# Performance work log

Hardware: AMD Instinct MI355X
Metric: run time of the kernel (lower is better)

The kernel has to match this reference:

```python
import jax, jax.numpy as jnp
import numpy as np

B, N, X, H = 128, 1023, 256, 256  # N = 2**(D+1)-1 perfect binary trees, root at 0


def _lin_init(key, out_d, in_d, scale=None):
    if scale is None:
        scale = 1.0 / np.sqrt(in_d)
    kw, kb = jax.random.split(key)
    W = jax.random.uniform(kw, (out_d, in_d), jnp.float32, -scale, scale)
    b = jax.random.uniform(kb, (out_d,), jnp.float32, -scale, scale)
    return W, b


def setup_inputs() -> dict:
    key = jax.random.key(0)
    ks = jax.random.split(key, 16)
    embed = jax.random.normal(ks[0], (B, N, X), jnp.float32)
    Wf, bf = _lin_init(ks[1], H, X + H)
    Wi, bi = _lin_init(ks[2], H, X + H)
    Wu, bu = _lin_init(ks[3], H, X + H)
    Wo, bo = _lin_init(ks[4], H, X + H)
    # extra nn.Parameter biases, initialized to zeros as in the module
    b_f = jnp.zeros((H,), jnp.float32)
    b_i = jnp.zeros((H,), jnp.float32)
    b_u = jnp.zeros((H,), jnp.float32)
    b_o = jnp.zeros((H,), jnp.float32)
    W1, bl1 = _lin_init(ks[5], H, H)
    W2, bl2 = _lin_init(ks[6], H, H)
    W3, bl3 = _lin_init(ks[7], H, H)
    W4, bl4 = _lin_init(ks[8], H, H)
    return {"embed": embed, "Wf": Wf, "bf": bf, "b_f": b_f, "Wi": Wi, "bi": bi,
            "b_i": b_i, "Wu": Wu, "bu": bu, "b_u": b_u, "Wo": Wo, "bo": bo,
            "b_o": b_o, "W1": W1, "bl1": bl1, "W2": W2, "bl2": bl2,
            "W3": W3, "bl3": bl3, "W4": W4, "bl4": bl4}


def _tree_lstm(embed, Wf, bf, b_f, Wi, bi, b_i, Wu, bu, b_u, Wo, bo, b_o):
    Bn, Nn, Xn = embed.shape
    Hn = Wf.shape[0]
    D = int(np.log2(Nn + 1)) - 1  # leaf level index
    h = jnp.zeros((Bn, Nn, Hn), embed.dtype)
    c = jnp.zeros((Bn, Nn, Hn), embed.dtype)
    # initial (leaf) level: no children -> h_sum = 0, c_tilde = 0 (apply_node_func on init state)
    i_g = jax.nn.sigmoid(bi + b_i)
    u_g = jnp.tanh(bu + b_u)
    c_leaf = i_g * u_g
    h_leaf = jax.nn.sigmoid(bo + b_o) * jnp.tanh(c_leaf)
    ls, lc = 2 ** D - 1, 2 ** D
    h = h.at[:, ls:ls + lc].set(jnp.broadcast_to(h_leaf, (Bn, lc, Hn)))
    c = c.at[:, ls:ls + lc].set(jnp.broadcast_to(c_leaf, (Bn, lc, Hn)))
    # level-by-level leaf->root; children of node n are 2n+1, 2n+2 (contiguous per level)
    for l in range(D - 1, -1, -1):
        s, cnt = 2 ** l - 1, 2 ** l
        cs, ccnt = 2 ** (l + 1) - 1, 2 ** (l + 1)
        ch_h = h[:, cs:cs + ccnt]        # [B, 2*cnt, H]
        ch_c = c[:, cs:cs + ccnt]
        ch_e = embed[:, cs:cs + ccnt]
        # message: cat([h, embed]); reduce: sum over the 2 children
        msg = jnp.concatenate([ch_h, ch_e], axis=-1).reshape(Bn, cnt, 2, Hn + Xn)
        h_sum = msg.sum(axis=2)                                   # [B, cnt, H+X]
        c_sum = ch_c.reshape(Bn, cnt, 2, Hn).sum(axis=2)          # [B, cnt, H]
        f = jax.nn.sigmoid(h_sum @ Wf.T + bf + b_f)
        c_tilde = f * c_sum  # f broadcast over children: f*(c1+c2) == sum_k f*c_k
        i_gate = jax.nn.sigmoid(h_sum @ Wi.T + bi + b_i)
        u = jnp.tanh(h_sum @ Wu.T + bu + b_u)
        c_new = i_gate * u + c_tilde
        o = jax.nn.sigmoid(h_sum @ Wo.T + bo + b_o)
        h_new = o * jnp.tanh(c_new)
        h = h.at[:, s:s + cnt].set(h_new)
        c = c.at[:, s:s + cnt].set(c_new)
    return h[:, 0]  # root hidden state, [B, H]


def reference(embed, Wf, bf, b_f, Wi, bi, b_i, Wu, bu, b_u, Wo, bo, b_o,
              W1, bl1, W2, bl2, W3, bl3, W4, bl4):
    hr = _tree_lstm(embed, Wf, bf, b_f, Wi, bi, b_i, Wu, bu, b_u, Wo, bo, b_o)
    # dropout is identity in eval mode
    y = jnp.tanh(hr @ W1.T + bl1)
    y2 = jax.nn.relu(hr @ W2.T + bl2) @ W3.T + bl3
    return jax.nn.relu((y + y2) @ W4.T + bl4)
```

## Files before the change

kernel.cpp:

```cpp
#include <hip/hip_runtime.h>

#define HD 256
#define KD 512

typedef _Float16 half8 __attribute__((ext_vector_type(8)));
typedef _Float16 half2v __attribute__((ext_vector_type(2)));
typedef _Float16 half4v __attribute__((ext_vector_type(4)));
typedef float floatx4 __attribute__((ext_vector_type(4)));
typedef float floatx2 __attribute__((ext_vector_type(2)));

__device__ __forceinline__ float sigmf_(float x) { return 1.f / (1.f + __expf(-x)); }
__device__ __forceinline__ float tanhf_(float x) {
  x = fminf(fmaxf(x, -15.f), 15.f);
  float e = __expf(2.f * x);
  return (e - 1.f) / (e + 1.f);
}

__global__ void prep_kernel(const float* __restrict__ bf_, const float* __restrict__ b_f,
                            const float* __restrict__ bi_, const float* __restrict__ b_i,
                            const float* __restrict__ bu_, const float* __restrict__ b_u,
                            const float* __restrict__ bo_, const float* __restrict__ b_o,
                            const float* __restrict__ Wf, const float* __restrict__ Wi,
                            const float* __restrict__ Wu, const float* __restrict__ Wo,
                            float* __restrict__ bsum, float* __restrict__ bias2,
                            float* __restrict__ cleaf2)
{
  __shared__ float hl2[HD];
  __shared__ float part[64][4];
  const int t = threadIdx.x;
  float sf = bf_[t] + b_f[t];
  float si = bi_[t] + b_i[t];
  float su = bu_[t] + b_u[t];
  float so = bo_[t] + b_o[t];
  float ig = 1.f / (1.f + expf(-si));
  float uu = tanhf(su);
  float cl = ig * uu;
  float hl = (1.f / (1.f + expf(-so))) * tanhf(cl);
  hl2[t] = 2.f * hl;
  if (blockIdx.x == 0) {
    bsum[t] = sf; bsum[HD + t] = si; bsum[2 * HD + t] = su; bsum[3 * HD + t] = so;
    cleaf2[t] = cl + cl;
  }
  __syncthreads();
  const int g = blockIdx.x >> 2, q = blockIdx.x & 3;
  const int nl = t >> 2, kq = t & 3;
  const float* Wg = (g == 0) ? Wf : (g == 1) ? Wi : (g == 2) ? Wu : Wo;
  const float* w = Wg + (long)(q * 64 + nl) * KD + kq * 64;
  float s = 0.f;
  for (int k = 0; k < 64; k += 4) {
    floatx4 wv = *(const floatx4*)(w + k);
    floatx4 hv = *(const floatx4*)(&hl2[kq * 64 + k]);
    s += wv[0] * hv[0] + wv[1] * hv[1] + wv[2] * hv[2] + wv[3] * hv[3];
  }
  part[nl][kq] = s;
  __syncthreads();
  if (kq == 0) {
    const int n = q * 64 + nl;
    float tot = part[nl][0] + part[nl][1] + part[nl][2] + part[nl][3];
    float bg = (g == 0) ? (bf_[n] + b_f[n]) : (g == 1) ? (bi_[n] + b_i[n])
             : (g == 2) ? (bu_[n] + b_u[n]) : (bo_[n] + b_o[n]);
    bias2[g * HD + n] = bg + tot;
  }
}

__global__ void wcvt_kernel(const float* __restrict__ Wf, const float* __restrict__ Wi,
                            const float* __restrict__ Wu, const float* __restrict__ Wo,
                            _Float16* __restrict__ Wh)
{
  int idx = (blockIdx.x * 256 + threadIdx.x) * 4;
  int g = idx >> 17;
  int rem = idx & ((1 << 17) - 1);
  const float* src = (g == 0) ? Wf : (g == 1) ? Wi : (g == 2) ? Wu : Wo;
  floatx4 v = *(const floatx4*)(src + rem);
  half4v o;
  o[0] = (_Float16)v[0]; o[1] = (_Float16)v[1]; o[2] = (_Float16)v[2]; o[3] = (_Float16)v[3];
  *(half4v*)(Wh + idx) = o;
}

__global__ void esum_kernel(const float* __restrict__ embed, _Float16* __restrict__ esum)
{
  const int task = blockIdx.x * 256 + threadIdx.x;
  if (task >= 511 * 32) return;
  const int b = blockIdx.y;
  const int p = task >> 5, g8 = task & 31;
  const float* e0 = embed + ((long)b * 1023 + 2 * p + 1) * 256 + g8 * 8;
  const float* e1 = e0 + 256;
  floatx4 x0 = *(const floatx4*)(e0);
  floatx4 x1 = *(const floatx4*)(e0 + 4);
  floatx4 y0 = *(const floatx4*)(e1);
  floatx4 y1 = *(const floatx4*)(e1 + 4);
  half8 s;
#pragma unroll
  for (int e = 0; e < 4; ++e) { s[e] = (_Float16)(x0[e] + y0[e]); s[4 + e] = (_Float16)(x1[e] + y1[e]); }
  *(half8*)(esum + ((long)b * 511 + p) * 256 + g8 * 8) = s;
}

__global__ __launch_bounds__(256, 2)
void level_kernel(const _Float16* __restrict__ hsum_in,
                  const float* __restrict__ csum_in,
                  const _Float16* __restrict__ esum,
                  const _Float16* __restrict__ Wh,
                  const float* __restrict__ bias,
                  _Float16* __restrict__ hsum_out,
                  float* __restrict__ csum_out,
                  int l, int leaf, int fin)
{
  __shared__ _Float16 As[128][256];

  const int cb = blockIdx.y;
  const int m0 = blockIdx.x * 128;
  const int t = threadIdx.x;
  const int wave = t >> 6;
  const int lane = t & 63;
  const int lm = lane & 15;
  const int quad = lane >> 4;
  const int rh = wave >> 1;
  const int ch = wave & 1;
  const int ncol = cb * 32 + ch * 16 + lm;

  floatx4 acc[4][4] = {};

  const int srow0 = t >> 3;
  const int sg = t & 7;

  const _Float16* wb = Wh + (long)ncol * KD + quad * 8;

  auto gemm_chunk = [&](int kbase) {
    half8 bcur[4], bnxt[4];
#pragma unroll
    for (int g = 0; g < 4; ++g)
      bcur[g] = *(const half8*)(wb + (long)g * HD * KD + kbase);
#pragma unroll
    for (int ks = 0; ks < 8; ++ks) {
      if (ks < 7) {
#pragma unroll
        for (int g = 0; g < 4; ++g)
          bnxt[g] = *(const half8*)(wb + (long)g * HD * KD + kbase + (ks + 1) * 32);
      }
      half8 afr[4];
#pragma unroll
      for (int mt = 0; mt < 4; ++mt) {
        int row = rh * 64 + mt * 16 + lm;
        afr[mt] = *(const half8*)(&As[row][(((ks * 4 + quad) ^ (row & 7)) * 8)]);
      }
#pragma unroll
      for (int mt = 0; mt < 4; ++mt)
#pragma unroll
        for (int g = 0; g < 4; ++g)
          acc[mt][g] = __builtin_amdgcn_mfma_f32_16x16x32_f16(afr[mt], bcur[g], acc[mt][g], 0, 0, 0);
#pragma unroll
      for (int g = 0; g < 4; ++g) bcur[g] = bnxt[g];
    }
  };

  const int msk = (1 << l) - 1;

  if (!leaf) {
#pragma unroll
    for (int p = 0; p < 4; ++p) {
      const int r = srow0 + 32 * p;
      const _Float16* src = hsum_in + (long)(m0 + r) * HD;
#pragma unroll
      for (int q = 0; q < 4; ++q) {
        int g8 = sg + 8 * q;
        *(half8*)(&As[r][((g8 ^ (r & 7)) * 8)]) = *(const half8*)(src + g8 * 8);
      }
    }
    __syncthreads();
    gemm_chunk(0);
    __syncthreads();
  }

  {
#pragma unroll
    for (int p = 0; p < 4; ++p) {
      const int r = srow0 + 32 * p;
      const int sm = m0 + r;
      const long erow = (long)(sm >> l) * 511 + msk + (sm & msk);
      const _Float16* src = esum + erow * HD;
#pragma unroll
      for (int q = 0; q < 4; ++q) {
        int g8 = sg + 8 * q;
        *(half8*)(&As[r][((g8 ^ (r & 7)) * 8)]) = *(const half8*)(src + g8 * 8);
      }
    }
  }
  __syncthreads();
  gemm_chunk(256);

  const float b0 = bias[ncol];
  const float b1 = bias[HD + ncol];
  const float b2 = bias[2 * HD + ncol];
  const float b3 = bias[3 * HD + ncol];
  const float clv = leaf ? csum_in[ncol] : 0.f;

#pragma unroll
  for (int mt = 0; mt < 4; ++mt) {
    const int mg0 = m0 + rh * 64 + mt * 16 + quad * 4;
    float hv[4], cvv[4];
#pragma unroll
    for (int e = 0; e < 4; ++e) {
      float cs = leaf ? clv : csum_in[(long)(mg0 + e) * HD + ncol];
      float zf = acc[mt][0][e] + b0;
      float zi = acc[mt][1][e] + b1;
      float zu = acc[mt][2][e] + b2;
      float zo = acc[mt][3][e] + b3;
      float f = sigmf_(zf), ig = sigmf_(zi), uu = tanhf_(zu), oo = sigmf_(zo);
      float cn = ig * uu + f * cs;
      cvv[e] = cn;
      hv[e] = oo * tanhf_(cn);
    }
    if (fin) {
#pragma unroll
      for (int e = 0; e < 4; ++e)
        hsum_out[(long)(mg0 + e) * HD + ncol] = (_Float16)hv[e];
    } else {
      const long pr = mg0 >> 1;
      hsum_out[pr * HD + ncol] = (_Float16)(hv[0] + hv[1]);
      hsum_out[(pr + 1) * HD + ncol] = (_Float16)(hv[2] + hv[3]);
      csum_out[pr * HD + ncol] = cvv[0] + cvv[1];
      csum_out[(pr + 1) * HD + ncol] = cvv[2] + cvv[3];
    }
  }
}

__global__ __launch_bounds__(256, 2)
void level_kernel_w(const _Float16* __restrict__ hsum_in,
                    const float* __restrict__ csum_in,
                    const _Float16* __restrict__ esum,
                    const _Float16* __restrict__ Wh,
                    const float* __restrict__ bias,
                    _Float16* __restrict__ hsum_out,
                    float* __restrict__ csum_out,
                    int l, int leaf)
{
  __shared__ _Float16 As[128][256];

  const int cb = blockIdx.y;
  const int m0 = blockIdx.x * 128;
  const int t = threadIdx.x;
  const int wave = t >> 6;
  const int lane = t & 63;
  const int lm = lane & 15;
  const int quad = lane >> 4;
  const int ncol = cb * 64 + wave * 16 + lm;

  floatx4 acc[8][4] = {};

  const int srow0 = t >> 3;
  const int sg = t & 7;

  const _Float16* wb = Wh + (long)ncol * KD + quad * 8;

  auto gemm_chunk = [&](int kbase) {
    half8 bcur[4], bnxt[4];
#pragma unroll
    for (int g = 0; g < 4; ++g)
      bcur[g] = *(const half8*)(wb + (long)g * HD * KD + kbase);
#pragma unroll
    for (int ks = 0; ks < 8; ++ks) {
      if (ks < 7) {
#pragma unroll
        for (int g = 0; g < 4; ++g)
          bnxt[g] = *(const half8*)(wb + (long)g * HD * KD + kbase + (ks + 1) * 32);
      }
      half8 afr[8];
#pragma unroll
      for (int mt = 0; mt < 8; ++mt) {
        int row = mt * 16 + lm;
        afr[mt] = *(const half8*)(&As[row][(((ks * 4 + quad) ^ (row & 7)) * 8)]);
      }
#pragma unroll
      for (int mt = 0; mt < 8; ++mt)
#pragma unroll
        for (int g = 0; g < 4; ++g)
          acc[mt][g] = __builtin_amdgcn_mfma_f32_16x16x32_f16(afr[mt], bcur[g], acc[mt][g], 0, 0, 0);
#pragma unroll
      for (int g = 0; g < 4; ++g) bcur[g] = bnxt[g];
    }
  };

  const int msk = (1 << l) - 1;

  if (!leaf) {
#pragma unroll
    for (int p = 0; p < 4; ++p) {
      const int r = srow0 + 32 * p;
      const _Float16* src = hsum_in + (long)(m0 + r) * HD;
#pragma unroll
      for (int q = 0; q < 4; ++q) {
        int g8 = sg + 8 * q;
        *(half8*)(&As[r][((g8 ^ (r & 7)) * 8)]) = *(const half8*)(src + g8 * 8);
      }
    }
    __syncthreads();
    gemm_chunk(0);
    __syncthreads();
  }

  {
#pragma unroll
    for (int p = 0; p < 4; ++p) {
      const int r = srow0 + 32 * p;
      const int sm = m0 + r;
      const long erow = (long)(sm >> l) * 511 + msk + (sm & msk);
      const _Float16* src = esum + erow * HD;
#pragma unroll
      for (int q = 0; q < 4; ++q) {
        int g8 = sg + 8 * q;
        *(half8*)(&As[r][((g8 ^ (r & 7)) * 8)]) = *(const half8*)(src + g8 * 8);
      }
    }
  }
  __syncthreads();
  gemm_chunk(256);

  const float b0 = bias[ncol];
  const float b1 = bias[HD + ncol];
  const float b2 = bias[2 * HD + ncol];
  const float b3 = bias[3 * HD + ncol];
  const float clv = leaf ? csum_in[ncol] : 0.f;

#pragma unroll
  for (int mt = 0; mt < 8; ++mt) {
    const int mg0 = m0 + mt * 16 + quad * 4;
    float hv[4], cvv[4];
#pragma unroll
    for (int e = 0; e < 4; ++e) {
      float cs = leaf ? clv : csum_in[(long)(mg0 + e) * HD + ncol];
      float zf = acc[mt][0][e] + b0;
      float zi = acc[mt][1][e] + b1;
      float zu = acc[mt][2][e] + b2;
      float zo = acc[mt][3][e] + b3;
      float f = sigmf_(zf), ig = sigmf_(zi), uu = tanhf_(zu), oo = sigmf_(zo);
      float cn = ig * uu + f * cs;
      cvv[e] = cn;
      hv[e] = oo * tanhf_(cn);
    }
    const long pr = mg0 >> 1;
    hsum_out[pr * HD + ncol] = (_Float16)(hv[0] + hv[1]);
    hsum_out[(pr + 1) * HD + ncol] = (_Float16)(hv[2] + hv[3]);
    csum_out[pr * HD + ncol] = cvv[0] + cvv[1];
    csum_out[(pr + 1) * HD + ncol] = cvv[2] + cvv[3];
  }
}

__global__ void head_all_kernel(const _Float16* __restrict__ hr,
                                const float* __restrict__ W1, const float* __restrict__ bl1,
                                const float* __restrict__ W2, const float* __restrict__ bl2,
                                const float* __restrict__ W3, const float* __restrict__ bl3,
                                const float* __restrict__ W4, const float* __restrict__ bl4,
                                float* __restrict__ out)
{
  __shared__ float a[HD];
  __shared__ float t1s[HD];
  __shared__ float t2s[HD];
  int b = blockIdx.x, n = threadIdx.x;
  a[n] = (float)hr[b * HD + n];
  __syncthreads();
  {
    const float* w1 = W1 + n * HD;
    const float* w2 = W2 + n * HD;
    float s1 = bl1[n], s2 = bl2[n];
    for (int k = 0; k < HD; k += 4) {
      floatx4 av = *(const floatx4*)(&a[k]);
      floatx4 w1v = *(const floatx4*)(w1 + k);
      floatx4 w2v = *(const floatx4*)(w2 + k);
#pragma unroll
      for (int e = 0; e < 4; ++e) { s1 += av[e] * w1v[e]; s2 += av[e] * w2v[e]; }
    }
    t1s[n] = tanhf_(s1);
    t2s[n] = fmaxf(s2, 0.f);
  }
  __syncthreads();
  {
    const float* w3 = W3 + n * HD;
    float s3 = bl3[n];
    for (int k = 0; k < HD; k += 4) {
      floatx4 av = *(const floatx4*)(&t2s[k]);
      floatx4 wv = *(const floatx4*)(w3 + k);
#pragma unroll
      for (int e = 0; e < 4; ++e) s3 += av[e] * wv[e];
    }
    __syncthreads();
    a[n] = t1s[n] + s3;
  }
  __syncthreads();
  {
    const float* w4 = W4 + n * HD;
    float s4 = bl4[n];
    for (int k = 0; k < HD; k += 4) {
      floatx4 av = *(const floatx4*)(&a[k]);
      floatx4 wv = *(const floatx4*)(w4 + k);
#pragma unroll
      for (int e = 0; e < 4; ++e) s4 += av[e] * wv[e];
    }
    out[b * HD + n] = fmaxf(s4, 0.f);
  }
}

extern "C" void kernel_launch(void* const* d_in, const int* in_sizes, int n_in,
                              void* d_out, int out_size, void* d_ws, size_t ws_size,
                              hipStream_t stream)
{
  (void)in_sizes; (void)n_in; (void)out_size; (void)ws_size;
  const float* embed = (const float*)d_in[0];
  const float* Wf  = (const float*)d_in[1];
  const float* bf_ = (const float*)d_in[2];
  const float* b_f = (const float*)d_in[3];
  const float* Wi  = (const float*)d_in[4];
  const float* bi_ = (const float*)d_in[5];
  const float* b_i = (const float*)d_in[6];
  const float* Wu  = (const float*)d_in[7];
  const float* bu_ = (const float*)d_in[8];
  const float* b_u = (const float*)d_in[9];
  const float* Wo  = (const float*)d_in[10];
  const float* bo_ = (const float*)d_in[11];
  const float* b_o = (const float*)d_in[12];
  const float* W1  = (const float*)d_in[13];
  const float* bl1 = (const float*)d_in[14];
  const float* W2  = (const float*)d_in[15];
  const float* bl2 = (const float*)d_in[16];
  const float* W3  = (const float*)d_in[17];
  const float* bl3 = (const float*)d_in[18];
  const float* W4  = (const float*)d_in[19];
  const float* bl4 = (const float*)d_in[20];

  char* ws = (char*)d_ws;
  _Float16* Wh   = (_Float16*)(ws);
  float* bsum    = (float*)(ws + 1048576);
  float* bias2   = (float*)(ws + 1052672);
  float* cleaf2  = (float*)(ws + 1056768);
  _Float16* hr   = (_Float16*)(ws + 1057792);
  _Float16* esum = (_Float16*)(ws + 1123328);
  _Float16* HsA  = (_Float16*)(ws + 34612224);
  float* CsA     = (float*)(ws + 43000832);
  _Float16* HsB  = (_Float16*)(ws + 59778048);
  float* CsB     = (float*)(ws + 63972352);

  prep_kernel<<<dim3(16), dim3(256), 0, stream>>>(bf_, b_f, bi_, b_i, bu_, b_u, bo_, b_o,
                                                  Wf, Wi, Wu, Wo, bsum, bias2, cleaf2);
  wcvt_kernel<<<dim3(512), dim3(256), 0, stream>>>(Wf, Wi, Wu, Wo, Wh);
  esum_kernel<<<dim3(64, 128), dim3(256), 0, stream>>>(embed, esum);

  _Float16* hbufs[2] = {HsA, HsB};
  float* cbufs[2] = {CsA, CsB};
  int pp = 0;
  const _Float16* hin = nullptr;
  const float* cin = cleaf2;
  for (int l = 8; l >= 0; --l) {
    const int leaf = (l == 8);
    const int fin = (l == 0);
    _Float16* hout = fin ? hr : hbufs[pp];
    float* cout = cbufs[pp];
    if (l >= 6) {
      dim3 grid(1 << l, 4);
      level_kernel_w<<<grid, dim3(256), 0, stream>>>(hin, cin, esum, Wh,
                                                     leaf ? bias2 : bsum,
                                                     hout, cout, l, leaf);
    } else {
      dim3 grid(1 << l, 8);
      level_kernel<<<grid, dim3(256), 0, stream>>>(hin, cin, esum, Wh,
                                                   leaf ? bias2 : bsum,
                                                   hout, cout, l, leaf, fin);
    }
    hin = hbufs[pp];
    cin = cbufs[pp];
    pp ^= 1;
  }

  head_all_kernel<<<dim3(128), dim3(256), 0, stream>>>(hr, W1, bl1, W2, bl2, W3, bl3,
                                                       W4, bl4, (float*)d_out);
}
```

Baseline: 463.3 us.

## Fuse upper tree levels into one cooperative kernel with grid syncs

New measurement: 748.6 us. 1.62x slower.

```diff
diff --git a/kernel.cpp b/kernel.cpp
--- a/kernel.cpp
+++ b/kernel.cpp
@@ -1,13 +1,14 @@
 #include <hip/hip_runtime.h>
+#include <hip/hip_cooperative_groups.h>
+
+namespace cg = cooperative_groups;
 
 #define HD 256
 #define KD 512
 
 typedef _Float16 half8 __attribute__((ext_vector_type(8)));
-typedef _Float16 half2v __attribute__((ext_vector_type(2)));
 typedef _Float16 half4v __attribute__((ext_vector_type(4)));
 typedef float floatx4 __attribute__((ext_vector_type(4)));
-typedef float floatx2 __attribute__((ext_vector_type(2)));
 
 __device__ __forceinline__ float sigmf_(float x) { return 1.f / (1.f + __expf(-x)); }
 __device__ __forceinline__ float tanhf_(float x) {
@@ -95,21 +96,15 @@
   *(half8*)(esum + ((long)b * 511 + p) * 256 + g8 * 8) = s;
 }
 
-__global__ __launch_bounds__(256, 2)
-void level_kernel(const _Float16* __restrict__ hsum_in,
-                  const float* __restrict__ csum_in,
-                  const _Float16* __restrict__ esum,
-                  const _Float16* __restrict__ Wh,
-                  const float* __restrict__ bias,
-                  _Float16* __restrict__ hsum_out,
-                  float* __restrict__ csum_out,
-                  int l, int leaf, int fin)
-{
-  __shared__ _Float16 As[128][256];
-
-  const int cb = blockIdx.y;
-  const int m0 = blockIdx.x * 128;
-  const int t = threadIdx.x;
+__device__ __forceinline__ void body_narrow(
+    _Float16 (*As)[256],
+    const _Float16* __restrict__ hsum_in, const float* __restrict__ csum_in,
+    const _Float16* __restrict__ esum, const _Float16* __restrict__ Wh,
+    const float* __restrict__ bias,
+    _Float16* __restrict__ hsum_out, float* __restrict__ csum_out,
+    int l, int fin, int bx, int cb, int t)
+{
+  const int m0 = bx * 128;
   const int wave = t >> 6;
   const int lane = t & 63;
   const int lm = lane & 15;
@@ -155,6 +150,122 @@
 
   const int msk = (1 << l) - 1;
 
+#pragma unroll
+  for (int p = 0; p < 4; ++p) {
+    const int r = srow0 + 32 * p;
+    const _Float16* src = hsum_in + (long)(m0 + r) * HD;
+#pragma unroll
+    for (int q = 0; q < 4; ++q) {
+      int g8 = sg + 8 * q;
+      *(half8*)(&As[r][((g8 ^ (r & 7)) * 8)]) = *(const half8*)(src + g8 * 8);
+    }
+  }
+  __syncthreads();
+  gemm_chunk(0);
+  __syncthreads();
+
+#pragma unroll
+  for (int p = 0; p < 4; ++p) {
+    const int r = srow0 + 32 * p;
+    const int sm = m0 + r;
+    const long erow = (long)(sm >> l) * 511 + msk + (sm & msk);
+    const _Float16* src = esum + erow * HD;
+#pragma unroll
+    for (int q = 0; q < 4; ++q) {
+      int g8 = sg + 8 * q;
+      *(half8*)(&As[r][((g8 ^ (r & 7)) * 8)]) = *(const half8*)(src + g8 * 8);
+    }
+  }
+  __syncthreads();
+  gemm_chunk(256);
+
+  const float b0 = bias[ncol];
+  const float b1 = bias[HD + ncol];
+  const float b2 = bias[2 * HD + ncol];
+  const float b3 = bias[3 * HD + ncol];
+
+#pragma unroll
+  for (int mt = 0; mt < 4; ++mt) {
+    const int mg0 = m0 + rh * 64 + mt * 16 + quad * 4;
+    float hv[4], cvv[4];
+#pragma unroll
+    for (int e = 0; e < 4; ++e) {
+      float cs = csum_in[(long)(mg0 + e) * HD + ncol];
+      float zf = acc[mt][0][e] + b0;
+      float zi = acc[mt][1][e] + b1;
+      float zu = acc[mt][2][e] + b2;
+      float zo = acc[mt][3][e] + b3;
+      float f = sigmf_(zf), ig = sigmf_(zi), uu = tanhf_(zu), oo = sigmf_(zo);
+      float cn = ig * uu + f * cs;
+      cvv[e] = cn;
+      hv[e] = oo * tanhf_(cn);
+    }
+    if (fin) {
+#pragma unroll
+      for (int e = 0; e < 4; ++e)
+        hsum_out[(long)(mg0 + e) * HD + ncol] = (_Float16)hv[e];
+    } else {
+      const long pr = mg0 >> 1;
+      hsum_out[pr * HD + ncol] = (_Float16)(hv[0] + hv[1]);
+      hsum_out[(pr + 1) * HD + ncol] = (_Float16)(hv[2] + hv[3]);
+      csum_out[pr * HD + ncol] = cvv[0] + cvv[1];
+      csum_out[(pr + 1) * HD + ncol] = cvv[2] + cvv[3];
+    }
+  }
+}
+
+__device__ __forceinline__ void body_wide(
+    _Float16 (*As)[256],
+    const _Float16* __restrict__ hsum_in, const float* __restrict__ csum_in,
+    const _Float16* __restrict__ esum, const _Float16* __restrict__ Wh,
+    const float* __restrict__ bias,
+    _Float16* __restrict__ hsum_out, float* __restrict__ csum_out,
+    int l, int leaf, int bx, int cb, int t)
+{
+  const int m0 = bx * 128;
+  const int wave = t >> 6;
+  const int lane = t & 63;
+  const int lm = lane & 15;
+  const int quad = lane >> 4;
+  const int ncol = cb * 64 + wave * 16 + lm;
+
+  floatx4 acc[8][4] = {};
+
+  const int srow0 = t >> 3;
+  const int sg = t & 7;
+
+  const _Float16* wb = Wh + (long)ncol * KD + quad * 8;
+
+  auto gemm_chunk = [&](int kbase) {
+    half8 bcur[4], bnxt[4];
+#pragma unroll
+    for (int g = 0; g < 4; ++g)
+      bcur[g] = *(const half8*)(wb + (long)g * HD * KD + kbase);
+#pragma unroll
+    for (int ks = 0; ks < 8; ++ks) {
+      if (ks < 7) {
+#pragma unroll
+        for (int g = 0; g < 4; ++g)
+          bnxt[g] = *(const half8*)(wb + (long)g * HD * KD + kbase + (ks + 1) * 32);
+      }
+      half8 afr[8];
+#pragma unroll
+      for (int mt = 0; mt < 8; ++mt) {
+        int row = mt * 16 + lm;
+        afr[mt] = *(const half8*)(&As[row][(((ks * 4 + quad) ^ (row & 7)) * 8)]);
+      }
+#pragma unroll
+      for (int mt = 0; mt < 8; ++mt)
+#pragma unroll
+        for (int g = 0; g < 4; ++g)
+          acc[mt][g] = __builtin_amdgcn_mfma_f32_16x16x32_f16(afr[mt], bcur[g], acc[mt][g], 0, 0, 0);
+#pragma unroll
+      for (int g = 0; g < 4; ++g) bcur[g] = bnxt[g];
+    }
+  };
+
+  const int msk = (1 << l) - 1;
+
   if (!leaf) {
 #pragma unroll
     for (int p = 0; p < 4; ++p) {
@@ -171,18 +282,16 @@
     __syncthreads();
   }
 
-  {
-#pragma unroll
-    for (int p = 0; p < 4; ++p) {
-      const int r = srow0 + 32 * p;
-      const int sm = m0 + r;
-      const long erow = (long)(sm >> l) * 511 + msk + (sm & msk);
-      const _Float16* src = esum + erow * HD;
-#pragma unroll
-      for (int q = 0; q < 4; ++q) {
-        int g8 = sg + 8 * q;
-        *(half8*)(&As[r][((g8 ^ (r & 7)) * 8)]) = *(const half8*)(src + g8 * 8);
-      }
+#pragma unroll
+  for (int p = 0; p < 4; ++p) {
+    const int r = srow0 + 32 * p;
+    const int sm = m0 + r;
+    const long erow = (long)(sm >> l) * 511 + msk + (sm & msk);
+    const _Float16* src = esum + erow * HD;
+#pragma unroll
+    for (int q = 0; q < 4; ++q) {
+      int g8 = sg + 8 * q;
+      *(half8*)(&As[r][((g8 ^ (r & 7)) * 8)]) = *(const half8*)(src + g8 * 8);
     }
   }
   __syncthreads();
@@ -195,8 +304,8 @@
   const float clv = leaf ? csum_in[ncol] : 0.f;
 
 #pragma unroll
-  for (int mt = 0; mt < 4; ++mt) {
-    const int mg0 = m0 + rh * 64 + mt * 16 + quad * 4;
+  for (int mt = 0; mt < 8; ++mt) {
+    const int mg0 = m0 + mt * 16 + quad * 4;
     float hv[4], cvv[4];
 #pragma unroll
     for (int e = 0; e < 4; ++e) {
@@ -210,17 +319,11 @@
       cvv[e] = cn;
       hv[e] = oo * tanhf_(cn);
     }
-    if (fin) {
-#pragma unroll
-      for (int e = 0; e < 4; ++e)
-        hsum_out[(long)(mg0 + e) * HD + ncol] = (_Float16)hv[e];
-    } else {
-      const long pr = mg0 >> 1;
-      hsum_out[pr * HD + ncol] = (_Float16)(hv[0] + hv[1]);
-      hsum_out[(pr + 1) * HD + ncol] = (_Float16)(hv[2] + hv[3]);
-      csum_out[pr * HD + ncol] = cvv[0] + cvv[1];
-      csum_out[(pr + 1) * HD + ncol] = cvv[2] + cvv[3];
-    }
+    const long pr = mg0 >> 1;
+    hsum_out[pr * HD + ncol] = (_Float16)(hv[0] + hv[1]);
+    hsum_out[(pr + 1) * HD + ncol] = (_Float16)(hv[2] + hv[3]);
+    csum_out[pr * HD + ncol] = cvv[0] + cvv[1];
+    csum_out[(pr + 1) * HD + ncol] = cvv[2] + cvv[3];
   }
 }
 
@@ -235,113 +338,46 @@
                     int l, int leaf)
 {
   __shared__ _Float16 As[128][256];
-
-  const int cb = blockIdx.y;
-  const int m0 = blockIdx.x * 128;
+  body_wide(As, hsum_in, csum_in, esum, Wh, bias, hsum_out, csum_out,
+            l, leaf, blockIdx.x, blockIdx.y, threadIdx.x);
+}
+
+__global__ __launch_bounds__(256, 2)
+void levels_tail_kernel(const _Float16* __restrict__ esum,
+                        const _Float16* __restrict__ Wh,
+                        const float* __restrict__ bsum,
+                        _Float16* __restrict__ HsA, float* __restrict__ CsA,
+                        _Float16* __restrict__ HsB, float* __restrict__ CsB,
+                        _Float16* __restrict__ hr)
+{
+  __shared__ _Float16 As[128][256];
+  cg::grid_group grid = cg::this_grid();
+  const int flat = blockIdx.x;
   const int t = threadIdx.x;
-  const int wave = t >> 6;
-  const int lane = t & 63;
-  const int lm = lane & 15;
-  const int quad = lane >> 4;
-  const int ncol = cb * 64 + wave * 16 + lm;
-
-  floatx4 acc[8][4] = {};
-
-  const int srow0 = t >> 3;
-  const int sg = t & 7;
-
-  const _Float16* wb = Wh + (long)ncol * KD + quad * 8;
-
-  auto gemm_chunk = [&](int kbase) {
-    half8 bcur[4], bnxt[4];
-#pragma unroll
-    for (int g = 0; g < 4; ++g)
-      bcur[g] = *(const half8*)(wb + (long)g * HD * KD + kbase);
-#pragma unroll
-    for (int ks = 0; ks < 8; ++ks) {
-      if (ks < 7) {
-#pragma unroll
-        for (int g = 0; g < 4; ++g)
-          bnxt[g] = *(const half8*)(wb + (long)g * HD * KD + kbase + (ks + 1) * 32);
-      }
-      half8 afr[8];
-#pragma unroll
-      for (int mt = 0; mt < 8; ++mt) {
-        int row = mt * 16 + lm;
-        afr[mt] = *(const half8*)(&As[row][(((ks * 4 + quad) ^ (row & 7)) * 8)]);
-      }
-#pragma unroll
-      for (int mt = 0; mt < 8; ++mt)
-#pragma unroll
-        for (int g = 0; g < 4; ++g)
-          acc[mt][g] = __builtin_amdgcn_mfma_f32_16x16x32_f16(afr[mt], bcur[g], acc[mt][g], 0, 0, 0);
-#pragma unroll
-      for (int g = 0; g < 4; ++g) bcur[g] = bnxt[g];
-    }
-  };
-
-  const int msk = (1 << l) - 1;
-
-  if (!leaf) {
-#pragma unroll
-    for (int p = 0; p < 4; ++p) {
-      const int r = srow0 + 32 * p;
-      const _Float16* src = hsum_in + (long)(m0 + r) * HD;
-#pragma unroll
-      for (int q = 0; q < 4; ++q) {
-        int g8 = sg + 8 * q;
-        *(half8*)(&As[r][((g8 ^ (r & 7)) * 8)]) = *(const half8*)(src + g8 * 8);
-      }
-    }
-    __syncthreads();
-    gemm_chunk(0);
-    __syncthreads();
-  }
-
-  {
-#pragma unroll
-    for (int p = 0; p < 4; ++p) {
-      const int r = srow0 + 32 * p;
-      const int sm = m0 + r;
-      const long erow = (long)(sm >> l) * 511 + msk + (sm & msk);
-      const _Float16* src = esum + erow * HD;
-#pragma unroll
-      for (int q = 0; q < 4; ++q) {
-        int g8 = sg + 8 * q;
-        *(half8*)(&As[r][((g8 ^ (r & 7)) * 8)]) = *(const half8*)(src + g8 * 8);
-      }
-    }
-  }
-  __syncthreads();
-  gemm_chunk(256);
-
-  const float b0 = bias[ncol];
-  const float b1 = bias[HD + ncol];
-  const float b2 = bias[2 * HD + ncol];
-  const float b3 = bias[3 * HD + ncol];
-  const float clv = leaf ? csum_in[ncol] : 0.f;
-
-#pragma unroll
-  for (int mt = 0; mt < 8; ++mt) {
-    const int mg0 = m0 + mt * 16 + quad * 4;
-    float hv[4], cvv[4];
-#pragma unroll
-    for (int e = 0; e < 4; ++e) {
-      float cs = leaf ? clv : csum_in[(long)(mg0 + e) * HD + ncol];
-      float zf = acc[mt][0][e] + b0;
-      float zi = acc[mt][1][e] + b1;
-      float zu = acc[mt][2][e] + b2;
-      float zo = acc[mt][3][e] + b3;
-      float f = sigmf_(zf), ig = sigmf_(zi), uu = tanhf_(zu), oo = sigmf_(zo);
-      float cn = ig * uu + f * cs;
-      cvv[e] = cn;
-      hv[e] = oo * tanhf_(cn);
-    }
-    const long pr = mg0 >> 1;
-    hsum_out[pr * HD + ncol] = (_Float16)(hv[0] + hv[1]);
-    hsum_out[(pr + 1) * HD + ncol] = (_Float16)(hv[2] + hv[3]);
-    csum_out[pr * HD + ncol] = cvv[0] + cvv[1];
-    csum_out[(pr + 1) * HD + ncol] = cvv[2] + cvv[3];
+
+  body_wide(As, HsB, CsB, esum, Wh, bsum, HsA, CsA,
+            6, 0, flat & 63, flat >> 6, t);
+  grid.sync();
+
+  _Float16* hbufs[2] = {HsA, HsB};
+  float* cbufs[2] = {CsA, CsB};
+  const _Float16* hin = HsA;
+  const float* cin = CsA;
+  int pp = 1;
+  for (int l = 5; l >= 0; --l) {
+    const int fin = (l == 0);
+    _Float16* hout = fin ? hr : hbufs[pp];
+    float* cout = cbufs[pp];
+    if (flat < (8 << l)) {
+      const int bx = flat & ((1 << l) - 1);
+      const int cb = flat >> l;
+      body_narrow(As, hin, cin, esum, Wh, bsum, hout, cout,
+                  l, fin, bx, cb, t);
+    }
+    grid.sync();
+    hin = hbufs[pp];
+    cin = cbufs[pp];
+    pp ^= 1;
   }
 }
 
@@ -443,30 +479,22 @@
   wcvt_kernel<<<dim3(512), dim3(256), 0, stream>>>(Wf, Wi, Wu, Wo, Wh);
   esum_kernel<<<dim3(64, 128), dim3(256), 0, stream>>>(embed, esum);
 
-  _Float16* hbufs[2] = {HsA, HsB};
-  float* cbufs[2] = {CsA, CsB};
-  int pp = 0;
-  const _Float16* hin = nullptr;
-  const float* cin = cleaf2;
-  for (int l = 8; l >= 0; --l) {
-    const int leaf = (l == 8);
-    const int fin = (l == 0);
-    _Float16* hout = fin ? hr : hbufs[pp];
-    float* cout = cbufs[pp];
-    if (l >= 6) {
-      dim3 grid(1 << l, 4);
-      level_kernel_w<<<grid, dim3(256), 0, stream>>>(hin, cin, esum, Wh,
-                                                     leaf ? bias2 : bsum,
-                                                     hout, cout, l, leaf);
-    } else {
-      dim3 grid(1 << l, 8);
-      level_kernel<<<grid, dim3(256), 0, stream>>>(hin, cin, esum, Wh,
-                                                   leaf ? bias2 : bsum,
-                                                   hout, cout, l, leaf, fin);
-    }
-    hin = hbufs[pp];
-    cin = cbufs[pp];
-    pp ^= 1;
+  level_kernel_w<<<dim3(256, 4), dim3(256), 0, stream>>>(nullptr, cleaf2, esum, Wh,
+                                                         bias2, HsA, CsA, 8, 1);
+  level_kernel_w<<<dim3(128, 4), dim3(256), 0, stream>>>(HsA, CsA, esum, Wh,
+                                                         bsum, HsB, CsB, 7, 0);
+  {
+    void* cargs[8];
+    cargs[0] = (void*)&esum;
+    cargs[1] = (void*)&Wh;
+    cargs[2] = (void*)&bsum;
+    cargs[3] = (void*)&HsA;
+    cargs[4] = (void*)&CsA;
+    cargs[5] = (void*)&HsB;
+    cargs[6] = (void*)&CsB;
+    cargs[7] = (void*)&hr;
+    hipLaunchCooperativeKernel((void*)levels_tail_kernel, dim3(256), dim3(256),
+                               cargs, 0, stream);
   }
 
   head_all_kernel<<<dim3(128), dim3(256), 0, stream>>>(hr, W1, bl1, W2, bl2, W3, bl3,
```
